# Performance work log

Hardware: AMD Instinct MI355X
Metric: run time of the kernel (lower is better)

The kernel has to match this reference:

```python
import jax, jax.numpy as jnp
import numpy as np

jax.config.update("jax_enable_x64", True)  # int64 pairing keys, as in the torch code

N_ATOMS = 50000
DEG_HALF = 16           # undirected edges per atom on average -> E = 2*N*16 = 1.6M
D_FEAT = 128
H_DIM = 64
KEY_SCALE = 1e10        # matches (10000000000 * x).long() in the original


def setup_inputs() -> dict:
    rng = np.random.default_rng(0)
    half = N_ATOMS * DEG_HALF
    c = rng.integers(0, N_ATOMS, half)
    n = rng.integers(0, N_ATOMS, half)
    n = np.where(n == c, (n + 1) % N_ATOMS, n)
    c[0], n[0] = N_ATOMS - 1, 0  # guarantee atom N-1 appears as a center
    # scale vectors so int64 keys have a wide range (avoids pairing-key collisions)
    v = (rng.standard_normal((half, 3)) * 50.0).astype(np.float32)
    center = np.concatenate([c, n])
    neigh = np.concatenate([n, c])
    vec = np.concatenate([v, -v], axis=0)  # reverse edge has negated vector, same length
    order = np.argsort(center, kind="stable")  # edge_center sorted -> edge_center[-1] is max
    center, neigh, vec = center[order], neigh[order], vec[order]
    lengths = np.linalg.norm(vec.astype(np.float64), axis=1).astype(np.float32)

    E = 2 * half
    k = jax.random.key(0)
    kf, k1, k2, k3, k4 = jax.random.split(k, 5)
    feats = jax.random.normal(kf, (E, D_FEAT), jnp.float32)
    w1 = jax.random.normal(k1, (D_FEAT, H_DIM), jnp.float32) / np.sqrt(D_FEAT)
    b1 = jax.random.normal(k2, (H_DIM,), jnp.float32) * 0.01
    w2 = jax.random.normal(k3, (H_DIM, 1), jnp.float32) / np.sqrt(H_DIM)
    b2 = jax.random.normal(k4, (1,), jnp.float32) * 0.01
    return {
        "features": feats,
        "edge_vectors": jnp.asarray(vec, jnp.float32),
        "edge_lengths": jnp.asarray(lengths, jnp.float32),
        "edge_index": jnp.asarray(np.stack([center, neigh]), jnp.int64),
        "w1": w1, "b1": b1, "w2": w2, "b2": b2,
    }


def _forward(features, edge_vectors, edge_lengths, edge_index, w1, b1, w2, b2):
    center = edge_index[0]
    neigh = edge_index[1]
    # per-edge MLP: Linear -> ShiftedSoftplus -> Linear(->1)
    ssp = lambda x: jax.nn.softplus(x) - jnp.log(2.0).astype(x.dtype)
    h = ssp(features @ w1 + b1)
    mag = h @ w2 + b2  # [E, 1]
    # scatter-mean debias per center atom
    ones = jnp.ones_like(mag[:, 0])
    cnt = jax.ops.segment_sum(ones, center, num_segments=N_ATOMS)
    bias = jax.ops.segment_sum(mag[:, 0], center, num_segments=N_ATOMS) / jnp.maximum(cnt, 1.0)
    mag = mag - bias[center][:, None]
    unit_vec = edge_vectors / edge_lengths[:, None]
    # ghost-atom branch: inputs are built so edge_neighbor <= max(edge_center); no ghosts.
    # sorted-pair averaging (no_grad key, E even -> argsort().view(-1, 2))
    ul = jax.lax.stop_gradient(edge_lengths)
    uv = jax.lax.stop_gradient(unit_vec)
    key_i = (center.astype(jnp.int64) + neigh.astype(jnp.int64)
             + (KEY_SCALE * ul).astype(jnp.int64)
             + (KEY_SCALE * jnp.abs(uv).sum(axis=1)).astype(jnp.int64))
    idx = jnp.argsort(key_i)
    pairs = idx.reshape(-1, 2)
    avg = 0.5 * (mag[pairs[:, 0]] + mag[pairs[:, 1]])
    mag = mag.at[pairs[:, 0]].set(avg).at[pairs[:, 1]].set(avg)
    edge_force = mag * unit_vec  # [E, 3]
    forces = jax.ops.segment_sum(edge_force, center, num_segments=N_ATOMS)
    return forces


def reference(features, edge_vectors, edge_lengths, edge_index, w1, b1, w2, b2):
    return _forward(features, edge_vectors, edge_lengths, edge_index, w1, b1, w2, b2)
```

## Files before the change

kernel.cpp:

```cpp
#include <hip/hip_runtime.h>

typedef __bf16 bf16x8 __attribute__((ext_vector_type(8)));
typedef float f32x4 __attribute__((ext_vector_type(4)));

#define DFEAT 128
#define HDIM 64
#define IDX_BITS 21
#define IDX_MASK ((1u << IDX_BITS) - 1)
#define EMPTY_SLOT 0xFFFFFFFFFFFFFFFFull

__device__ __forceinline__ float ssp_fast(float x) {
    float m = fmaxf(x, 0.0f);
    float t = __expf(-fabsf(x));
    return m + __logf(1.0f + t) - 0.69314718055994531f;
}

__global__ void detect_idx_kernel(const unsigned int* __restrict__ p, int n_check,
                                  unsigned int* __restrict__ flag_any) {
    unsigned int acc = 0;
    for (int i = threadIdx.x; i < n_check; i += blockDim.x)
        acc |= p[2 * i + 1];
    if (acc) atomicOr(flag_any, 1u);
}

__device__ __forceinline__ int load_idx(const void* p, int is64, long long i) {
    if (is64) return (int)((const long long*)p)[i];
    return ((const int*)p)[i];
}

#define CVT8H(P, Q, H) do { \
    H[0] = (__bf16)P.x; H[1] = (__bf16)P.y; H[2] = (__bf16)P.z; H[3] = (__bf16)P.w; \
    H[4] = (__bf16)Q.x; H[5] = (__bf16)Q.y; H[6] = (__bf16)Q.z; H[7] = (__bf16)Q.w; \
} while (0)

#define MF(A, B, C) __builtin_amdgcn_mfma_f32_16x16x32_bf16(A, B, C, 0, 0, 0)

#define KSTEP(P, Q, KT) do { \
    bf16x8 h, bh; \
    CVT8H(P, Q, h); \
    bh = hiTab[((KT)*4 + 0) * 64 + lane]; acc0 = MF(h, bh, acc0); \
    bh = hiTab[((KT)*4 + 1) * 64 + lane]; acc1 = MF(h, bh, acc1); \
    bh = hiTab[((KT)*4 + 2) * 64 + lane]; acc2 = MF(h, bh, acc2); \
    bh = hiTab[((KT)*4 + 3) * 64 + lane]; acc3 = MF(h, bh, acc3); \
} while (0)

#define REDJ(J, OUT) do { \
    float z0 = acc0[J] + b1v0, z1 = acc1[J] + b1v1; \
    float z2 = acc2[J] + b1v2, z3 = acc3[J] + b1v3; \
    float t = ssp_fast(z0) * w2v0 + ssp_fast(z1) * w2v1 \
            + ssp_fast(z2) * w2v2 + ssp_fast(z3) * w2v3; \
    t += __shfl_xor(t, 1); t += __shfl_xor(t, 2); \
    t += __shfl_xor(t, 4); t += __shfl_xor(t, 8); \
    OUT = t; \
} while (0)

__global__ __launch_bounds__(256, 4) void mlp_mag_kernel(
    const float* __restrict__ feats,
    const float* __restrict__ w1,
    const float* __restrict__ b1,
    const float* __restrict__ w2,
    const float* __restrict__ b2,
    float* __restrict__ mag_raw,
    int E)
{
    __shared__ __align__(16) unsigned char smem[32768];
    float* w1s = (float*)smem;
    bf16x8* hiTab = (bf16x8*)smem;

    const int lane = threadIdx.x & 63;
    const int r = lane & 15;
    const int g = lane >> 4;
    const int wave = blockIdx.x * (blockDim.x >> 6) + (threadIdx.x >> 6);
    const int nwaves = gridDim.x * (blockDim.x >> 6);

    for (int idx = threadIdx.x; idx < DFEAT * HDIM / 4; idx += blockDim.x)
        ((float4*)w1s)[idx] = ((const float4*)w1)[idx];
    __syncthreads();
    {
        const int tkt = threadIdx.x >> 6;
        const int tl = threadIdx.x & 63;
        const int tg = tl >> 4, tr = tl & 15;
        float vals[4][8];
#pragma unroll
        for (int nt = 0; nt < 4; ++nt)
#pragma unroll
            for (int i = 0; i < 8; ++i)
                vals[nt][i] = w1s[(tkt * 32 + tg * 8 + i) * HDIM + nt * 16 + tr];
        __syncthreads();
#pragma unroll
        for (int nt = 0; nt < 4; ++nt) {
            bf16x8 h;
#pragma unroll
            for (int i = 0; i < 8; ++i) h[i] = (__bf16)vals[nt][i];
            hiTab[(tkt * 4 + nt) * 64 + tl] = h;
        }
        __syncthreads();
    }

    const float b1v0 = b1[0 * 16 + r], b1v1 = b1[1 * 16 + r];
    const float b1v2 = b1[2 * 16 + r], b1v3 = b1[3 * 16 + r];
    const float w2v0 = w2[0 * 16 + r], w2v1 = w2[1 * 16 + r];
    const float w2v2 = w2[2 * 16 + r], w2v3 = w2[3 * 16 + r];
    const float b2v = b2[0];

    const int ntiles = (E + 15) >> 4;
    for (int tile = wave; tile < ntiles; tile += nwaves) {
        const int e0 = tile << 4;
        int er = e0 + r;
        if (er >= E) er = E - 1;

        const float4* fp = (const float4*)(feats + (size_t)er * DFEAT) + g * 2;
        float4 p0 = fp[0],  p1 = fp[1];
        float4 p2 = fp[8],  p3 = fp[9];
        float4 p4 = fp[16], p5 = fp[17];
        float4 p6 = fp[24], p7 = fp[25];

        f32x4 acc0 = {0.f,0.f,0.f,0.f}, acc1 = {0.f,0.f,0.f,0.f};
        f32x4 acc2 = {0.f,0.f,0.f,0.f}, acc3 = {0.f,0.f,0.f,0.f};
        KSTEP(p0, p1, 0);
        KSTEP(p2, p3, 1);
        KSTEP(p4, p5, 2);
        KSTEP(p6, p7, 3);

        float s0, s1, s2, s3;
        REDJ(0, s0); REDJ(1, s1); REDJ(2, s2); REDJ(3, s3);

        if (r < 4) {
            int e = e0 + g * 4 + r;
            if (e < E) {
                float sel = (r == 0) ? s0 : (r == 1) ? s1 : (r == 2) ? s2 : s3;
                mag_raw[e] = sel + b2v;
            }
        }
    }
}

__global__ __launch_bounds__(256) void bias_kernel(
    const void* __restrict__ eidx,
    const float* __restrict__ mag,
    float* __restrict__ csum,
    float* __restrict__ ccnt,
    const unsigned int* __restrict__ flag_any,
    int E)
{
    __shared__ int cs[256];
    __shared__ float ms[256];
    const int is64 = (flag_any[0] == 0u) ? 1 : 0;
    const int tloc = threadIdx.x;
    const int i = blockIdx.x * 256 + tloc;
    int c = -1; float m = 0.0f;
    if (i < E) { c = load_idx(eidx, is64, i); m = mag[i]; }
    cs[tloc] = c; ms[tloc] = m;
    __syncthreads();
    if (i < E) {
        bool leader = (tloc == 0) || (cs[tloc - 1] != c);
        if (leader) {
            float s = 0.0f; int n = 0; int j = tloc;
            int lim = min(256, E - blockIdx.x * 256);
            while (j < lim && cs[j] == c) { s += ms[j]; ++n; ++j; }
            atomicAdd(&csum[c], s);
            atomicAdd(&ccnt[c], (float)n);
        }
    }
}

__global__ __launch_bounds__(256) void pair_kernel(
    const float* __restrict__ vec,
    const float* __restrict__ len,
    const void* __restrict__ eidx,
    float* __restrict__ mag,
    const float* __restrict__ csum,
    const float* __restrict__ ccnt,
    unsigned long long* __restrict__ tab,
    const unsigned int* __restrict__ flag_any,
    int E, int hash_bits)
{
    int i = blockIdx.x * blockDim.x + threadIdx.x;
    if (i >= E) return;
    const int is64 = (flag_any[0] == 0u) ? 1 : 0;

    float l = len[i];
    float ux = vec[3 * i + 0] / l;
    float uy = vec[3 * i + 1] / l;
    float uz = vec[3 * i + 2] / l;
    float s3 = (fabsf(ux) + fabsf(uy)) + fabsf(uz);

    int ci_ = load_idx(eidx, is64, i);
    int ni_ = load_idx(eidx, is64, (long long)E + i);

    long long key = (long long)ci_ + (long long)ni_
                  + (long long)(1.0e10f * l)
                  + (long long)(1.0e10f * s3);

    unsigned long long entry = ((unsigned long long)key << IDX_BITS) | (unsigned)i;
    unsigned long long h = (unsigned long long)key * 0x9E3779B97F4A7C15ull;
    unsigned slot = (unsigned)(h >> (64 - hash_bits));
    const unsigned smask = (1u << hash_bits) - 1u;

    int j;
    while (true) {
        unsigned long long old = atomicCAS(&tab[slot], EMPTY_SLOT, entry);
        if (old == EMPTY_SLOT) return;
        if ((old >> IDX_BITS) == (unsigned long long)key) {
            j = (int)(old & IDX_MASK);
            break;
        }
        slot = (slot + 1) & smask;
    }

    int cj_ = load_idx(eidx, is64, j);
    float mi = mag[i] - csum[ci_] / fmaxf(ccnt[ci_], 1.0f);
    float mj = mag[j] - csum[cj_] / fmaxf(ccnt[cj_], 1.0f);
    float avg = 0.5f * (mi + mj);
    mag[i] = avg;
    mag[j] = avg;
}

__global__ __launch_bounds__(256) void force_kernel(
    const float* __restrict__ vec,
    const float* __restrict__ len,
    const void* __restrict__ eidx,
    const float* __restrict__ mag,
    float* __restrict__ out,
    const unsigned int* __restrict__ flag_any,
    int E)
{
    __shared__ int cs[256];
    __shared__ float fx[256], fy[256], fz[256];
    const int is64 = (flag_any[0] == 0u) ? 1 : 0;
    const int tloc = threadIdx.x;
    const int i = blockIdx.x * 256 + tloc;
    int c = -1;
    if (i < E) {
        c = load_idx(eidx, is64, i);
        float l = len[i];
        float m = mag[i];
        fx[tloc] = m * vec[3 * i + 0] / l;
        fy[tloc] = m * vec[3 * i + 1] / l;
        fz[tloc] = m * vec[3 * i + 2] / l;
    }
    cs[tloc] = c;
    __syncthreads();
    if (i < E) {
        bool leader = (tloc == 0) || (cs[tloc - 1] != c);
        if (leader) {
            float sx = 0.f, sy = 0.f, sz = 0.f;
            int j = tloc;
            int lim = min(256, E - blockIdx.x * 256);
            while (j < lim && cs[j] == c) { sx += fx[j]; sy += fy[j]; sz += fz[j]; ++j; }
            atomicAdd(&out[c * 3 + 0], sx);
            atomicAdd(&out[c * 3 + 1], sy);
            atomicAdd(&out[c * 3 + 2], sz);
        }
    }
}

extern "C" void kernel_launch(void* const* d_in, const int* in_sizes, int n_in,
                              void* d_out, int out_size, void* d_ws, size_t ws_size,
                              hipStream_t stream) {
    const float* feats = (const float*)d_in[0];
    const float* vec   = (const float*)d_in[1];
    const float* len   = (const float*)d_in[2];
    const void*  eidx  = d_in[3];
    const float* w1 = (const float*)d_in[4];
    const float* b1 = (const float*)d_in[5];
    const float* w2 = (const float*)d_in[6];
    const float* b2 = (const float*)d_in[7];
    float* out = (float*)d_out;

    const int E = in_sizes[0] / DFEAT;
    const int N = out_size / 3;

    char* ws = (char*)d_ws;
    size_t off_mag  = 0;
    size_t off_csum = (off_mag + (size_t)E * 4 + 255) & ~(size_t)255;
    size_t off_ccnt = off_csum + (size_t)N * 4;
    size_t off_flag = (off_ccnt + (size_t)N * 4 + 255) & ~(size_t)255;
    size_t off_tab  = off_flag + 256;

    float* mag     = (float*)(ws + off_mag);
    float* csum    = (float*)(ws + off_csum);
    float* ccnt    = (float*)(ws + off_ccnt);
    unsigned int* flag_any = (unsigned int*)(ws + off_flag);

    int hash_bits = 21;
    while (hash_bits > 20 && off_tab + (8ull << hash_bits) > ws_size) --hash_bits;
    unsigned long long* tab = (unsigned long long*)(ws + off_tab);

    hipMemsetAsync(csum, 0, off_flag + 256 - off_csum, stream);
    hipMemsetAsync(tab, 0xFF, (size_t)8 << hash_bits, stream);
    hipMemsetAsync(out, 0, (size_t)out_size * 4, stream);

    int n_check = E < 1024 ? E : 1024;
    detect_idx_kernel<<<1, 256, 0, stream>>>((const unsigned int*)eidx, n_check, flag_any);

    mlp_mag_kernel<<<1024, 256, 0, stream>>>(feats, w1, b1, w2, b2, mag, E);

    int eblocks = (E + 255) / 256;
    bias_kernel<<<eblocks, 256, 0, stream>>>(eidx, mag, csum, ccnt, flag_any, E);
    pair_kernel<<<eblocks, 256, 0, stream>>>(vec, len, eidx, mag, csum, ccnt,
                                             tab, flag_any, E, hash_bits);
    force_kernel<<<eblocks, 256, 0, stream>>>(vec, len, eidx, mag, out, flag_any, E);
}
```

Baseline: 335.4 us.

## Fuse pair averaging and force scatter into one kernel with per-pair atomics

Merges the pairing kernel and the force reduction kernel. Once an edge finds its partner in the hash table, it computes the averaged magnitude and scatters the force to both centers with atomics, using the negated unit vector for the partner. This removes the write-back of mag and the extra full pass over the vectors, lengths and indices. The cost is six scattered float atomics per pair in place of a segmented in-block reduction with few atomics. It also assumes the partner edge's unit vector is exactly the negation.

```diff
diff --git a/kernel.cpp b/kernel.cpp
--- a/kernel.cpp
+++ b/kernel.cpp
@@ -164,14 +164,15 @@
     }
 }
 
-__global__ __launch_bounds__(256) void pair_kernel(
+__global__ __launch_bounds__(256) void pair_force_kernel(
     const float* __restrict__ vec,
     const float* __restrict__ len,
     const void* __restrict__ eidx,
-    float* __restrict__ mag,
+    const float* __restrict__ mag,
     const float* __restrict__ csum,
     const float* __restrict__ ccnt,
     unsigned long long* __restrict__ tab,
+    float* __restrict__ out,
     const unsigned int* __restrict__ flag_any,
     int E, int hash_bits)
 {
@@ -209,50 +210,17 @@
     }
 
     int cj_ = load_idx(eidx, is64, j);
-    float mi = mag[i] - csum[ci_] / fmaxf(ccnt[ci_], 1.0f);
-    float mj = mag[j] - csum[cj_] / fmaxf(ccnt[cj_], 1.0f);
-    float avg = 0.5f * (mi + mj);
-    mag[i] = avg;
-    mag[j] = avg;
-}
-
-__global__ __launch_bounds__(256) void force_kernel(
-    const float* __restrict__ vec,
-    const float* __restrict__ len,
-    const void* __restrict__ eidx,
-    const float* __restrict__ mag,
-    float* __restrict__ out,
-    const unsigned int* __restrict__ flag_any,
-    int E)
-{
-    __shared__ int cs[256];
-    __shared__ float fx[256], fy[256], fz[256];
-    const int is64 = (flag_any[0] == 0u) ? 1 : 0;
-    const int tloc = threadIdx.x;
-    const int i = blockIdx.x * 256 + tloc;
-    int c = -1;
-    if (i < E) {
-        c = load_idx(eidx, is64, i);
-        float l = len[i];
-        float m = mag[i];
-        fx[tloc] = m * vec[3 * i + 0] / l;
-        fy[tloc] = m * vec[3 * i + 1] / l;
-        fz[tloc] = m * vec[3 * i + 2] / l;
-    }
-    cs[tloc] = c;
-    __syncthreads();
-    if (i < E) {
-        bool leader = (tloc == 0) || (cs[tloc - 1] != c);
-        if (leader) {
-            float sx = 0.f, sy = 0.f, sz = 0.f;
-            int j = tloc;
-            int lim = min(256, E - blockIdx.x * 256);
-            while (j < lim && cs[j] == c) { sx += fx[j]; sy += fy[j]; sz += fz[j]; ++j; }
-            atomicAdd(&out[c * 3 + 0], sx);
-            atomicAdd(&out[c * 3 + 1], sy);
-            atomicAdd(&out[c * 3 + 2], sz);
-        }
-    }
+    float bi = csum[ci_] / fmaxf(ccnt[ci_], 1.0f);
+    float bj = csum[cj_] / fmaxf(ccnt[cj_], 1.0f);
+    float avg = 0.5f * ((mag[i] - bi) + (mag[j] - bj));
+
+    float fx = avg * ux, fy = avg * uy, fz = avg * uz;
+    atomicAdd(&out[ci_ * 3 + 0], fx);
+    atomicAdd(&out[ci_ * 3 + 1], fy);
+    atomicAdd(&out[ci_ * 3 + 2], fz);
+    atomicAdd(&out[cj_ * 3 + 0], -fx);
+    atomicAdd(&out[cj_ * 3 + 1], -fy);
+    atomicAdd(&out[cj_ * 3 + 2], -fz);
 }
 
 extern "C" void kernel_launch(void* const* d_in, const int* in_sizes, int n_in,
@@ -298,7 +266,6 @@
 
     int eblocks = (E + 255) / 256;
     bias_kernel<<<eblocks, 256, 0, stream>>>(eidx, mag, csum, ccnt, flag_any, E);
-    pair_kernel<<<eblocks, 256, 0, stream>>>(vec, len, eidx, mag, csum, ccnt,
-                                             tab, flag_any, E, hash_bits);
-    force_kernel<<<eblocks, 256, 0, stream>>>(vec, len, eidx, mag, out, flag_any, E);
-}
+    pair_force_kernel<<<eblocks, 256, 0, stream>>>(vec, len, eidx, mag, csum, ccnt,
+                                                   tab, out, flag_any, E, hash_bits);
+}
```

New measurement: 583.1 us. +73.9%, slower.
